# Performance work log

Measured on AMD Instinct MI355X. Metric: run time of the kernel, lower is better.

Reference implementation:

```python
import jax, jax.numpy as jnp
import numpy as np

B, T = 64, 512
E, F, NUM = 8, 64, 16          # num embedding features, per-feature emb dim, numeric feats
D = E * F + NUM                 # 528, input_dim
HE = 512                        # encoder_hidden
HD = 512                        # decoder_gru_hidden
V = 500                         # vocab per categorical feature


def setup_inputs() -> dict:
    key = jax.random.key(0)
    ks = jax.random.split(key, 32)
    se = 1.0 / np.sqrt(HE)
    sd = 1.0 / np.sqrt(HD)
    u = lambda k, shape, s: jax.random.uniform(k, shape, jnp.float32, -s, s)
    return dict(
        x=jax.random.normal(ks[0], (B, T, D), jnp.float32),
        # encoder nn.GRU params (gate order r,z,n)
        Wih=u(ks[1], (3 * HE, D), se), Whh=u(ks[2], (3 * HE, HE), se),
        bih=u(ks[3], (3 * HE,), se), bhh=u(ks[4], (3 * HE,), se),
        # decoder layer 0 (input_size=D)
        W0x=u(ks[5], (3 * HD, D), sd), b0x=u(ks[6], (3 * HD,), sd),
        W0h=u(ks[7], (3 * HD, HD), sd), b0h=u(ks[8], (3 * HD,), sd),
        W0m=u(ks[9], (HD, HE + HD), sd), b0m=u(ks[10], (HD,), sd),
        # decoder layer 1 (input_size=HD)
        W1x=u(ks[11], (3 * HD, HD), sd), b1x=u(ks[12], (3 * HD,), sd),
        W1h=u(ks[13], (3 * HD, HD), sd), b1h=u(ks[14], (3 * HD,), sd),
        W1m=u(ks[15], (HD, HE + HD), sd), b1m=u(ks[16], (HD,), sd),
        # output heads
        Wout=u(ks[17], (D, HD), sd), bout=u(ks[18], (D,), sd),
        Wdel=u(ks[19], (1, HD), sd), bdel=u(ks[20], (1,), sd),
        # stacked per-feature vocab heads: Linear(F, V) for each of E features
        Wemb=u(ks[21], (E, V, F), 1.0 / np.sqrt(F)), bemb=u(ks[22], (E, V), 1.0 / np.sqrt(F)),
        seq_lens=jax.random.randint(ks[23], (B,), 1, T + 1),
    )


def _gru_cell(xg, hg, hx):
    # xg, hg: [B, 3H] precomputed input/hidden projections; hx: mixed hidden
    xr, xz, xn = jnp.split(xg, 3, axis=-1)
    hr, hz, hn = jnp.split(hg, 3, axis=-1)
    r = jax.nn.sigmoid(xr + hr)
    z = jax.nn.sigmoid(xz + hz)
    n = jnp.tanh(xn + r * hn)
    return z * hx + (1.0 - z) * n  # custom GRUCell convention: hy = z*hx + (1-z)*n


def reference(x, Wih, Whh, bih, bhh, W0x, b0x, W0h, b0h, W0m, b0m,
              W1x, b1x, W1h, b1h, W1m, b1m, Wout, bout, Wdel, bdel,
              Wemb, bemb, seq_lens):
    Bc, Tc, Dc = x.shape
    # ---------------- encoder: standard nn.GRU ----------------
    xg_enc = jnp.einsum('btd,gd->tbg', x, Wih) + bih  # [T,B,3HE]

    def enc_step(h, xt):
        hg = h @ Whh.T + bhh
        xr, xz, xn = jnp.split(xt, 3, axis=-1)
        hr, hz, hn = jnp.split(hg, 3, axis=-1)
        r = jax.nn.sigmoid(xr + hr)
        z = jax.nn.sigmoid(xz + hz)
        n = jnp.tanh(xn + r * hn)
        h = (1.0 - z) * n + z * h  # torch nn.GRU convention
        return h, h

    _, hs = jax.lax.scan(enc_step, jnp.zeros((Bc, HE), x.dtype), xg_enc)  # hs: [T,B,HE]
    lens = jnp.clip(seq_lens - 1, 0, Tc - 1)
    last_hidden = hs[lens, jnp.arange(Bc)]  # == all_hid[:, lens].diagonal().T -> [B,HE]

    # ---------------- DecoderGRU with per-step global mixing ----------------
    x2h0 = jnp.einsum('btd,gd->tbg', x, W0x) + b0x  # [T,B,3HD]
    # mix_global(cat([global_hidden, hx])) : global part is constant over time
    ghm0 = last_hidden @ W0m[:, :HE].T + b0m  # [B,HD]
    ghm1 = last_hidden @ W1m[:, :HE].T + b1m
    W0mh = W0m[:, HE:]
    W1mh = W1m[:, HE:]

    def dec_step(carry, xg_t):
        h0, h1 = carry
        hx0 = ghm0 + h0 @ W0mh.T
        h0 = _gru_cell(xg_t, hx0 @ W0h.T + b0h, hx0)
        xg1 = h0 @ W1x.T + b1x
        hx1 = ghm1 + h1 @ W1mh.T
        h1 = _gru_cell(xg1, hx1 @ W1h.T + b1h, hx1)
        return (h0, h1), h1

    z0 = jnp.zeros((Bc, HD), x.dtype)
    _, dec = jax.lax.scan(dec_step, (z0, z0), x2h0)  # [T,B,HD]
    dec = dec.transpose(1, 0, 2)  # [B,T,HD]

    out = (dec @ Wout.T + bout)[:, :-1, :]              # [B,T-1,D]
    pred_delta = (dec @ Wdel.T + bdel)[:, :-1, 0]       # [B,T-1]
    resized = out[:, :, :E * F].reshape(Bc, Tc - 1, E, F)
    emb_logits = jnp.einsum('btef,evf->ebtv', resized, Wemb) + bemb[:, None, None, :]
    return out, pred_delta, emb_logits, last_hidden
```

## Files before the change

### kernel.cpp

```cpp
#include <hip/hip_runtime.h>
#include <stdint.h>

typedef unsigned short u16;
typedef __attribute__((ext_vector_type(8))) short short8;
typedef __attribute__((ext_vector_type(4))) float f32x4;

#define MFMA16(a,b,c) __builtin_amdgcn_mfma_f32_16x16x32_bf16((a),(b),(c),0,0,0)
#define AT_LD(p)    __hip_atomic_load((p), __ATOMIC_RELAXED, __HIP_MEMORY_SCOPE_AGENT)
#define AT_ST(p,v)  __hip_atomic_store((p), (v), __ATOMIC_RELAXED, __HIP_MEMORY_SCOPE_AGENT)

__device__ __forceinline__ float b2f(u16 u){
  union { uint32_t i; float f; } v; v.i = ((uint32_t)u) << 16; return v.f;
}
__device__ __forceinline__ u16 f2bf(float f){
  union { float f; uint32_t i; } v; v.f = f;
  uint32_t x = v.i;
  return (u16)((x + 0x7fffu + ((x >> 16) & 1u)) >> 16);
}
__device__ __forceinline__ float sigm(float x){ return 1.f/(1.f + __expf(-x)); }
__device__ __forceinline__ float tanh_f(float x){ float e = __expf(-2.f*x); return 2.f/(1.f+e) - 1.f; }

__device__ __forceinline__ void gbar_arrive(unsigned* flags, int my, unsigned target){
  __syncthreads();
  if (threadIdx.x == 0) AT_ST(&flags[my*32], target);
}
__device__ __forceinline__ void gbar_wait32(unsigned* flags, unsigned target){
  if (threadIdx.x < 32){
    while (AT_LD(&flags[threadIdx.x*32]) < target) {}
  }
  __syncthreads();
}
__device__ __forceinline__ void gbar_wait64(unsigned* flags, unsigned target){
  if (threadIdx.x < 64){
    while (AT_LD(&flags[threadIdx.x*32]) < target) {}
  }
  __syncthreads();
}

__device__ __forceinline__ f32x4 xpose4(f32x4 a, int m){
  int b0 = m & 1, b1 = (m >> 1) & 1;
  float s01 = b0 ? a[0] : a[1];
  float s23 = b0 ? a[2] : a[3];
  float r01 = __shfl_xor(s01, 1);
  float r23 = __shfl_xor(s23, 1);
  float w0 = b0 ? r01 : a[0];
  float w1 = b0 ? a[1] : r01;
  float w2 = b0 ? r23 : a[2];
  float w3 = b0 ? a[3] : r23;
  float u02 = b1 ? w0 : w2;
  float u13 = b1 ? w1 : w3;
  float p02 = __shfl_xor(u02, 2);
  float p13 = __shfl_xor(u13, 2);
  f32x4 x;
  x[0] = b1 ? p02 : w0;
  x[1] = b1 ? p13 : w1;
  x[2] = b1 ? w2 : p02;
  x[3] = b1 ? w3 : p13;
  return x;
}

__global__ void cvt_pad(const float* __restrict__ src, u16* __restrict__ dst,
                        int R, int sStride, int sOff, int Cd, int Ccopy){
  int i = blockIdx.x*256 + threadIdx.x;
  if (i >= R*Cd) return;
  int r = i / Cd, c = i % Cd;
  dst[i] = (c < Ccopy) ? f2bf(src[(size_t)r*sStride + sOff + c]) : (u16)0;
}

__global__ void padf(const float* __restrict__ src, float* __restrict__ dst, int R, int Cs, int Cd){
  int i = blockIdx.x*256 + threadIdx.x;
  if (i >= R*Cd) return;
  int r = i/Cd, c = i%Cd;
  dst[i] = (c < Cs) ? src[r*Cs + c] : 0.f;
}

__global__ void wmT_kernel(const float* __restrict__ Wm, u16* __restrict__ dst){
  int idx = blockIdx.x*256 + threadIdx.x;
  if (idx >= 512*512) return;
  int j = idx >> 9, k = idx & 511;
  dst[idx] = f2bf(Wm[(size_t)k*1024 + 512 + j]);
}

__global__ __launch_bounds__(256) void gemm_bt(
    const u16* __restrict__ A, int lda,
    const u16* __restrict__ Bw, int ldb,
    const float* __restrict__ bias,
    int M, int N, int K, int mode,
    void* __restrict__ o0, void* __restrict__ o1, void* __restrict__ o2, int ldo)
{
  if (mode == 3){
    int e = blockIdx.z;
    A    += (size_t)e * 64;
    Bw   += (size_t)e * 512 * 64;
    bias += (size_t)e * 512;
  }
  __shared__ u16 As[128*64];
  __shared__ u16 Bs[128*64];
  const int row0 = blockIdx.x * 128, col0 = blockIdx.y * 128;
  const int tid = threadIdx.x;
  const int l = tid & 63, w = tid >> 6;
  const int lr = l & 15, lk = l >> 4;
  const int wr = w >> 1, wc = w & 1;
  f32x4 acc[4][4];
  #pragma unroll
  for (int a=0;a<4;++a)
    #pragma unroll
    for (int b=0;b<4;++b) acc[a][b] = (f32x4){0.f,0.f,0.f,0.f};

  for (int k0 = 0; k0 < K; k0 += 64){
    #pragma unroll
    for (int s = 0; s < 4; ++s){
      int cid = s*256 + tid;
      int r = cid >> 3, ck = cid & 7;
      *(short8*)&As[r*64 + ck*8] = *(const short8*)&A[(size_t)(row0 + r)*lda + k0 + ck*8];
      *(short8*)&Bs[r*64 + ck*8] = *(const short8*)&Bw[(size_t)(col0 + r)*ldb + k0 + ck*8];
    }
    __syncthreads();
    #pragma unroll
    for (int kt = 0; kt < 2; ++kt){
      short8 af[4], bf[4];
      #pragma unroll
      for (int mt=0;mt<4;++mt) af[mt] = *(const short8*)&As[(wr*64 + mt*16 + lr)*64 + kt*32 + lk*8];
      #pragma unroll
      for (int nt=0;nt<4;++nt) bf[nt] = *(const short8*)&Bs[(wc*64 + nt*16 + lr)*64 + kt*32 + lk*8];
      #pragma unroll
      for (int mt=0;mt<4;++mt)
        #pragma unroll
        for (int nt=0;nt<4;++nt) acc[mt][nt] = MFMA16(af[mt], bf[nt], acc[mt][nt]);
    }
    __syncthreads();
  }

  #pragma unroll
  for (int mt=0;mt<4;++mt){
    #pragma unroll
    for (int nt=0;nt<4;++nt){
      int col = col0 + wc*64 + nt*16 + lr;
      float bv = bias[col];
      #pragma unroll
      for (int i=0;i<4;++i){
        int r = row0 + wr*64 + mt*16 + lk*4 + i;
        float v = acc[mt][nt][i] + bv;
        if (mode == 0){
          int bb = r >> 9, t = r & 511;
          size_t ro = ((size_t)t*64 + bb)*1536;
          if (col < 1536) ((u16*)o0)[ro + col] = f2bf(v);
          else            ((u16*)o1)[ro + col - 1536] = f2bf(v);
        } else if (mode == 1){
          ((u16*)o0)[(size_t)r*ldo + col] = f2bf(v);
        } else if (mode == 2){
          int t = r >> 6, bb = r & 63;
          if (t < 511){
            size_t orow = (size_t)bb*511 + t;
            if (col < 512){
              ((float*)o0)[orow*528 + col] = v;
              ((u16*)o2)[orow*512 + col] = f2bf(v);
            } else if (col < 528){
              ((float*)o0)[orow*528 + col] = v;
            } else if (col == 528){
              ((float*)o1)[orow] = v;
            }
          }
        } else if (mode == 3){
          if (r < M && col < 500) ((float*)o0)[(size_t)(blockIdx.z)*16352000ull + (size_t)r*500 + col] = v;
        } else {
          if (r < M) ((float*)o0)[(size_t)r*ldo + col] = v;
        }
      }
    }
  }
}

__global__ __launch_bounds__(256,1) void enc_kernel(
    const u16* __restrict__ Whh, const float* __restrict__ bhh,
    const u16* __restrict__ XGE, const int* __restrict__ seqs,
    u16* __restrict__ hd, float* __restrict__ lasth,
    unsigned* __restrict__ flags)
{
  __shared__ u16 hs[64*512];
  const int tid = threadIdx.x;
  const int l = tid & 63, w = tid >> 6;
  const int lr = l & 15, lk = l >> 4;
  const int m = l & 3;
  const int gw = blockIdx.x*4 + w;
  const int hcol = gw*4 + (lr >> 2);

  const int msel = (m == 3) ? 0 : m;
  const u16* wbase = Whh + ((size_t)(msel*512) + hcol)*512;
  short8 bw[16];
  #pragma unroll
  for (int kt=0;kt<16;++kt) bw[kt] = *(const short8*)&wbase[kt*32 + lk*8];

  const float bhr = bhh[hcol], bhz = bhh[512+hcol], bhn = bhh[1024+hcol];
  int rowc[4]; int len[4]; float hreg[4];
  float xr[4], xz[4], xn[4];
  #pragma unroll
  for (int c=0;c<4;++c){
    rowc[c] = c*16 + lk*4 + m;
    len[c] = seqs[rowc[c]];
    hreg[c] = 0.f;
    const u16* p = XGE + (size_t)rowc[c]*1536;
    xr[c]=b2f(p[hcol]); xz[c]=b2f(p[512+hcol]); xn[c]=b2f(p[1024+hcol]);
  }

  for (int t=0; t<512; ++t){
    const u16* hrd = hd + (t & 1)*32768;
    u16*       hwr = hd + ((t & 1)^1)*32768;
    const unsigned* h32 = (const unsigned*)hrd;
    #pragma unroll
    for (int cc=0; cc<16; ++cc){
      int S = cc*256 + tid;
      int row = S >> 6, s = S & 63;
      union { unsigned u[4]; short8 v; } pk;
      #pragma unroll
      for (int j=0;j<4;++j) pk.u[j] = AT_LD(h32 + S*4 + j);
      *(short8*)&hs[row*512 + ((s ^ (row&7))<<3)] = pk.v;
    }
    __syncthreads();
    #pragma unroll
    for (int c=0;c<4;++c){
      short8 af[16];
      #pragma unroll
      for (int kt=0;kt<16;++kt)
        af[kt] = *(const short8*)&hs[(c*16+lr)*512 + (((kt*4+lk) ^ (lr&7))<<3)];
      f32x4 acc = (f32x4){0.f,0.f,0.f,0.f};
      #pragma unroll
      for (int kt=0;kt<16;++kt) acc = MFMA16(af[kt], bw[kt], acc);
      f32x4 x = xpose4(acc, m);
      float rg = sigm(xr[c] + x[0] + bhr);
      float zg = sigm(xz[c] + x[1] + bhz);
      float ng = tanh_f(xn[c] + rg*(x[2] + bhn));
      float hv = (1.f - zg)*ng + zg*hreg[c];
      hreg[c] = hv;
      AT_ST(&hwr[rowc[c]*512 + hcol], f2bf(hv));
      if (t == len[c]-1) lasth[rowc[c]*512 + hcol] = hv;
    }
    if (t < 511){
      gbar_arrive(flags, blockIdx.x, (unsigned)(t+1));
      const u16* xgn = XGE + (size_t)(t+1)*98304;
      #pragma unroll
      for (int c=0;c<4;++c){
        const u16* p = xgn + (size_t)rowc[c]*1536;
        xr[c]=b2f(p[hcol]); xz[c]=b2f(p[512+hcol]); xn[c]=b2f(p[1024+hcol]);
      }
      gbar_wait32(flags, (unsigned)(t+1));
    }
  }
}

__global__ __launch_bounds__(256,1) void decf_kernel(
    const u16* __restrict__ Wm0, const u16* __restrict__ Wcp0,
    const float* __restrict__ ghm0v, const float* __restrict__ ghW0v,
    const u16* __restrict__ W1xc, const float* __restrict__ b1xv,
    const u16* __restrict__ Wm1, const u16* __restrict__ Wcp1,
    const float* __restrict__ ghm1v, const float* __restrict__ ghW1v,
    const u16* __restrict__ XG0,
    u16* __restrict__ h0d, u16* __restrict__ h1d,
    u16* __restrict__ xgb,
    u16* __restrict__ Hall,
    unsigned* __restrict__ flags)
{
  __shared__ u16 hs[64*512];
  const int tid = threadIdx.x;
  const int l = tid & 63, w = tid >> 6;
  const int lr = l & 15, lk = l >> 4;
  const int m = l & 3;
  const int role1 = (blockIdx.x >= 32) ? 1 : 0;
  const int b = blockIdx.x & 31;
  const int gw = b*4 + w;
  const int hcol = gw*4 + (lr >> 2);

  const u16* Wm  = role1 ? Wm1  : Wm0;
  const u16* Wcp = role1 ? Wcp1 : Wcp0;
  const float* ghm = role1 ? ghm1v : ghm0v;
  const float* ghW = role1 ? ghW1v : ghW0v;
  u16* hd = role1 ? h1d : h0d;

  const u16* wb = (m == 0) ? (Wm + (size_t)hcol*512)
                           : (Wcp + ((size_t)((m-1)*512) + hcol)*512);
  short8 bw[16];
  #pragma unroll
  for (int kt=0;kt<16;++kt) bw[kt] = *(const short8*)&wb[kt*32 + lk*8];

  const bool xact = (!role1) && (gw < 96);
  const int xcol0 = gw*16;
  const int cbase = xcol0 + (lr & ~3);
  short8 bwx[16];
  float bx0=0.f, bx1=0.f, bx2=0.f, bx3=0.f;
  if (xact){
    #pragma unroll
    for (int kt=0;kt<16;++kt) bwx[kt] = *(const short8*)&W1xc[(size_t)(xcol0+lr)*512 + kt*32 + lk*8];
    bx0 = b1xv[cbase]; bx1 = b1xv[cbase+1]; bx2 = b1xv[cbase+2]; bx3 = b1xv[cbase+3];
  }

  int rowc[4]; float ghmr[4], g0[4], g1[4], g2[4];
  #pragma unroll
  for (int c=0;c<4;++c){
    int row = c*16 + lk*4 + m; rowc[c] = row;
    ghmr[c] = ghm[row*512 + hcol];
    g0[c] = ghW[row*1536 + hcol];
    g1[c] = ghW[row*1536 + 512 + hcol];
    g2[c] = ghW[row*1536 + 1024 + hcol];
  }
  float xr[4], xz[4], xn[4];
  if (!role1){
    #pragma unroll
    for (int c=0;c<4;++c){
      const u16* p = XG0 + (size_t)rowc[c]*1536;
      xr[c]=b2f(p[hcol]); xz[c]=b2f(p[512+hcol]); xn[c]=b2f(p[1024+hcol]);
    }
  } else {
    #pragma unroll
    for (int c=0;c<4;++c){ xr[c]=0.f; xz[c]=0.f; xn[c]=0.f; }
  }

  for (int p=0; p<=513; ++p){
    if (!role1){
      if (p <= 512){
        const int sp = p & 1;
        const u16* hrd = h0d + sp*32768;
        u16*       hwr = h0d + (sp^1)*32768;
        const unsigned* h32 = (const unsigned*)hrd;
        #pragma unroll
        for (int cc=0; cc<16; ++cc){
          int S = cc*256 + tid;
          int row = S >> 6, s = S & 63;
          union { unsigned u[4]; short8 v; } pk;
          #pragma unroll
          for (int j=0;j<4;++j) pk.u[j] = AT_LD(h32 + S*4 + j);
          *(short8*)&hs[row*512 + ((s ^ (row&7))<<3)] = pk.v;
        }
        __syncthreads();
        u16* xw = xgb + (size_t)((p-1)&1)*98304;
        #pragma unroll
        for (int c=0;c<4;++c){
          short8 af[16];
          #pragma unroll
          for (int kt=0;kt<16;++kt)
            af[kt] = *(const short8*)&hs[(c*16+lr)*512 + (((kt*4+lk) ^ (lr&7))<<3)];
          if (p <= 511){
            f32x4 ga = (f32x4){0.f,0.f,0.f,0.f};
            #pragma unroll
            for (int kt=0;kt<16;++kt) ga = MFMA16(af[kt], bw[kt], ga);
            f32x4 x = xpose4(ga, m);
            float hx = x[0] + ghmr[c];
            float rv = sigm(xr[c] + x[1] + g0[c]);
            float zv = sigm(xz[c] + x[2] + g1[c]);
            float nv = tanh_f(xn[c] + rv*(x[3] + g2[c]));
            float hv = zv*hx + (1.f - zv)*nv;
            AT_ST(&hwr[rowc[c]*512 + hcol], f2bf(hv));
          }
          if (p >= 1 && xact){
            f32x4 xa = (f32x4){0.f,0.f,0.f,0.f};
            #pragma unroll
            for (int kt=0;kt<16;++kt) xa = MFMA16(af[kt], bwx[kt], xa);
            f32x4 xv = xpose4(xa, m);
            unsigned lo = (unsigned)f2bf(xv[0]+bx0) | ((unsigned)f2bf(xv[1]+bx1) << 16);
            unsigned hi = (unsigned)f2bf(xv[2]+bx2) | ((unsigned)f2bf(xv[3]+bx3) << 16);
            unsigned long long v64 = (unsigned long long)lo | ((unsigned long long)hi << 32);
            __hip_atomic_store((unsigned long long*)&xw[(size_t)rowc[c]*1536 + cbase], v64,
                               __ATOMIC_RELAXED, __HIP_MEMORY_SCOPE_AGENT);
          }
        }
      }
    } else {
      if (p >= 2){
        const int t = p - 2;
        const u16* xb = xgb + (size_t)(t&1)*98304;
        #pragma unroll
        for (int c=0;c<4;++c){
          xr[c] = b2f(AT_LD(&xb[(size_t)rowc[c]*1536 + hcol]));
          xz[c] = b2f(AT_LD(&xb[(size_t)rowc[c]*1536 + 512 + hcol]));
          xn[c] = b2f(AT_LD(&xb[(size_t)rowc[c]*1536 + 1024 + hcol]));
        }
        const u16* hrd = h1d + (t&1)*32768;
        u16*       hwr = h1d + ((t&1)^1)*32768;
        const unsigned* h32 = (const unsigned*)hrd;
        #pragma unroll
        for (int cc=0; cc<16; ++cc){
          int S = cc*256 + tid;
          int row = S >> 6, s = S & 63;
          union { unsigned u[4]; short8 v; } pk;
          #pragma unroll
          for (int j=0;j<4;++j) pk.u[j] = AT_LD(h32 + S*4 + j);
          *(short8*)&hs[row*512 + ((s ^ (row&7))<<3)] = pk.v;
        }
        __syncthreads();
        #pragma unroll
        for (int c=0;c<4;++c){
          short8 af[16];
          #pragma unroll
          for (int kt=0;kt<16;++kt)
            af[kt] = *(const short8*)&hs[(c*16+lr)*512 + (((kt*4+lk) ^ (lr&7))<<3)];
          f32x4 ga = (f32x4){0.f,0.f,0.f,0.f};
          #pragma unroll
          for (int kt=0;kt<16;++kt) ga = MFMA16(af[kt], bw[kt], ga);
          f32x4 x = xpose4(ga, m);
          float hx = x[0] + ghmr[c];
          float rv = sigm(xr[c] + x[1] + g0[c]);
          float zv = sigm(xz[c] + x[2] + g1[c]);
          float nv = tanh_f(xn[c] + rv*(x[3] + g2[c]));
          float hv = zv*hx + (1.f - zv)*nv;
          u16 hb = f2bf(hv);
          AT_ST(&hwr[rowc[c]*512 + hcol], hb);
          Hall[(size_t)t*32768 + rowc[c]*512 + hcol] = hb;
        }
      }
    }
    if (p < 513){
      gbar_arrive(flags, blockIdx.x, (unsigned)(p+1));
      if (!role1 && p <= 510){
        const u16* xgn = XG0 + (size_t)(p+1)*98304;
        #pragma unroll
        for (int c=0;c<4;++c){
          const u16* q = xgn + (size_t)rowc[c]*1536;
          xr[c]=b2f(q[hcol]); xz[c]=b2f(q[512+hcol]); xn[c]=b2f(q[1024+hcol]);
        }
      }
      gbar_wait64(flags, (unsigned)(p+1));
    }
  }
}

__global__ void ghm_kernel(const float* __restrict__ lasth,
                           const float* __restrict__ W0m, const float* __restrict__ b0m,
                           const float* __restrict__ W1m, const float* __restrict__ b1m,
                           float* __restrict__ ghm0, float* __restrict__ ghm1,
                           u16* __restrict__ ghmP)
{
  int idx = blockIdx.x*256 + threadIdx.x;
  int chain = idx >> 15;
  int j = (idx >> 6) & 511;
  int b = idx & 63;
  const float* Wm = chain ? W1m : W0m;
  const float* bm = chain ? b1m : b0m;
  float s = 0.f;
  for (int k=0;k<512;++k) s += lasth[b*512 + k] * Wm[(size_t)j*1024 + k];
  float v = s + bm[j];
  (chain ? ghm1 : ghm0)[b*512 + j] = v;
  ghmP[(size_t)chain*65536 + b*512 + j] = f2bf(v);
}

extern "C" void kernel_launch(void* const* d_in, const int* in_sizes, int n_in,
                              void* d_out, int out_size, void* d_ws, size_t ws_size,
                              hipStream_t stream)
{
  const float* x    = (const float*)d_in[0];
  const float* Wih  = (const float*)d_in[1];
  const float* Whh  = (const float*)d_in[2];
  const float* bih  = (const float*)d_in[3];
  const float* bhh  = (const float*)d_in[4];
  const float* W0x  = (const float*)d_in[5];
  const float* b0x  = (const float*)d_in[6];
  const float* W0h  = (const float*)d_in[7];
  const float* b0h  = (const float*)d_in[8];
  const float* W0m  = (const float*)d_in[9];
  const float* b0m  = (const float*)d_in[10];
  const float* W1x  = (const float*)d_in[11];
  const float* b1x  = (const float*)d_in[12];
  const float* W1h  = (const float*)d_in[13];
  const float* b1h  = (const float*)d_in[14];
  const float* W1m  = (const float*)d_in[15];
  const float* b1m  = (const float*)d_in[16];
  const float* Wout = (const float*)d_in[17];
  const float* bout = (const float*)d_in[18];
  const float* Wdel = (const float*)d_in[19];
  const float* bdel = (const float*)d_in[20];
  const float* Wemb = (const float*)d_in[21];
  const float* bemb = (const float*)d_in[22];
  const int*   seqs = (const int*)d_in[23];
  float* out = (float*)d_out;

  const size_t OFF_DELTA = 17267712ull;
  const size_t OFF_EMB   = 17300416ull;
  const size_t OFF_LASTH = 148116416ull;

  uint8_t* ws = (uint8_t*)d_ws;
  size_t off = 0;
  auto alloc = [&](size_t bytes)->size_t{ size_t p = off; off += (bytes + 511) & ~(size_t)511; return p; };
  u16*   XGE  = (u16*)(ws + alloc(32768ull*1536*2));
  u16*   WmT0 = XGE;
  u16*   WmT1 = XGE + 262144;
  u16*   XG0  = (u16*)(ws + alloc(32768ull*1536*2));
  u16*   Ob   = XG0;
  uint8_t* reg3 = ws + alloc(2ull*33554432);
  u16*   Xp   = (u16*)reg3;
  u16*   H1   = (u16*)reg3;
  u16*   Wc   = (u16*)(ws + alloc(3072ull*576*2));
  u16*   Whc  = (u16*)(ws + alloc(1536ull*512*2));
  u16*   W0hc = (u16*)(ws + alloc(1536ull*512*2));
  u16*   W1hc = (u16*)(ws + alloc(1536ull*512*2));
  u16*   W1xc = (u16*)(ws + alloc(1536ull*512*2));
  u16*   Wm0c = (u16*)(ws + alloc(512ull*512*2));
  u16*   Wm1c = (u16*)(ws + alloc(512ull*512*2));
  u16*   Wcp0 = (u16*)(ws + alloc(1536ull*512*2));
  u16*   Wcp1 = (u16*)(ws + alloc(1536ull*512*2));
  u16*   Woc  = (u16*)(ws + alloc(640ull*512*2));
  u16*   Wep  = (u16*)(ws + alloc(8ull*512*64*2));
  u16*   ghmP = (u16*)(ws + alloc(2ull*128*512*2));
  u16*   xgb  = (u16*)(ws + alloc(2ull*64*1536*2));
  float* bc1  = (float*)(ws + alloc(3072*4));
  float* bc3  = (float*)(ws + alloc(640*4));
  float* bep  = (float*)(ws + alloc(8*512*4));
  float* bzero= (float*)(ws + alloc(512*4));
  float* ghm0 = (float*)(ws + alloc(64*512*4));
  float* ghm1 = (float*)(ws + alloc(64*512*4));
  float* ghW0 = (float*)(ws + alloc(64*1536*4));
  float* ghW1 = (float*)(ws + alloc(64*1536*4));
  size_t state_off = off;
  u16*   henc = (u16*)(ws + alloc(2*64*512*2));
  u16*   h0d  = (u16*)(ws + alloc(2*64*512*2));
  u16*   h1d  = (u16*)(ws + alloc(2*64*512*2));
  unsigned* bars = (unsigned*)(ws + alloc(16384));
  size_t state_bytes = off - state_off;
  if (ws_size < off) return;

  hipMemsetAsync(ws + state_off, 0, state_bytes, stream);
  hipMemsetAsync(Woc, 0, 640ull*512*2, stream);
  hipMemsetAsync(Wep, 0, 8ull*512*64*2, stream);
  hipMemsetAsync(ghmP, 0, 2ull*128*512*2, stream);
  hipMemsetAsync(bc3, 0, 640*4, stream);
  hipMemsetAsync(bzero, 0, 512*4, stream);

  hipMemcpyAsync(bc1,        bih,  1536*4, hipMemcpyDeviceToDevice, stream);
  hipMemcpyAsync(bc1 + 1536, b0x,  1536*4, hipMemcpyDeviceToDevice, stream);
  hipMemcpyAsync(bc3,        bout, 528*4,  hipMemcpyDeviceToDevice, stream);
  hipMemcpyAsync(bc3 + 528,  bdel, 4,      hipMemcpyDeviceToDevice, stream);

  auto CV = [&](const float* s, u16* d, int R, int sStride, int sOff, int Cd, int Ccopy){
    int total = R*Cd; int gb = (total + 255)/256;
    cvt_pad<<<dim3(gb), dim3(256), 0, stream>>>(s, d, R, sStride, sOff, Cd, Ccopy);
  };
  CV(x,    Xp, 32768, 528, 0, 576, 528);
  CV(Wih,  Wc,              1536, 528, 0, 576, 528);
  CV(W0x,  Wc + 1536ull*576,1536, 528, 0, 576, 528);
  CV(Whh,  Whc,  1536, 512, 0, 512, 512);
  CV(W0h,  W0hc, 1536, 512, 0, 512, 512);
  CV(W1h,  W1hc, 1536, 512, 0, 512, 512);
  CV(W1x,  W1xc, 1536, 512, 0, 512, 512);
  CV(W0m,  Wm0c, 512, 1024, 512, 512, 512);
  CV(W1m,  Wm1c, 512, 1024, 512, 512, 512);
  CV(Wout, Woc,              528, 512, 0, 512, 512);
  CV(Wdel, Woc + 528ull*512, 1,   512, 0, 512, 512);
  for (int e=0;e<8;++e) CV(Wemb + (size_t)e*32000, Wep + (size_t)e*32768, 500, 64, 0, 64, 64);
  {
    int gb = (8*512 + 255)/256;
    padf<<<dim3(gb), dim3(256), 0, stream>>>(bemb, bep, 8, 500, 512);
  }
  wmT_kernel<<<dim3(1024), dim3(256), 0, stream>>>(W0m, WmT0);
  wmT_kernel<<<dim3(1024), dim3(256), 0, stream>>>(W1m, WmT1);

  gemm_bt<<<dim3(12,4), dim3(256), 0, stream>>>(W0hc, 512, WmT0, 512, bzero,
      1536, 512, 512, 1, Wcp0, nullptr, nullptr, 512);
  gemm_bt<<<dim3(12,4), dim3(256), 0, stream>>>(W1hc, 512, WmT1, 512, bzero,
      1536, 512, 512, 1, Wcp1, nullptr, nullptr, 512);

  gemm_bt<<<dim3(256,24), dim3(256), 0, stream>>>(Xp, 576, Wc, 576, bc1,
      32768, 3072, 576, 0, XGE, XG0, nullptr, 0);
  enc_kernel<<<dim3(32), dim3(256), 0, stream>>>(Whc, bhh, XGE, seqs,
      henc, out + OFF_LASTH, bars + 0);
  ghm_kernel<<<dim3(256), dim3(256), 0, stream>>>(out + OFF_LASTH, W0m, b0m, W1m, b1m,
      ghm0, ghm1, ghmP);
  gemm_bt<<<dim3(1,12), dim3(256), 0, stream>>>(ghmP, 512, W0hc, 512, b0h,
      64, 1536, 512, 5, ghW0, nullptr, nullptr, 1536);
  gemm_bt<<<dim3(1,12), dim3(256), 0, stream>>>(ghmP + 65536, 512, W1hc, 512, b1h,
      64, 1536, 512, 5, ghW1, nullptr, nullptr, 1536);
  decf_kernel<<<dim3(64), dim3(256), 0, stream>>>(
      Wm0c, Wcp0, ghm0, ghW0, W1xc, b1x,
      Wm1c, Wcp1, ghm1, ghW1,
      XG0, h0d, h1d, xgb, H1, bars + 1024);
  gemm_bt<<<dim3(256,5), dim3(256), 0, stream>>>(H1, 512, Woc, 512, bc3,
      32768, 640, 512, 2, out, out + OFF_DELTA, Ob, 0);
  gemm_bt<<<dim3(256,4,8), dim3(256), 0, stream>>>(Ob, 512, Wep, 64, bep,
      32704, 512, 64, 3, out + OFF_EMB, nullptr, nullptr, 0);
}
```

Baseline: 9.492 ms.

## Halve persistent recurrent blocks with 512 threads to cut grid-barrier participants

The encoder and decoder recurrent kernels now run 16/32 blocks of 512 threads (8 waves each) instead of 32/64 blocks of 256, so each global barrier polls half as many flags. Hidden-state staging into LDS uses 64-bit atomic loads through a shared helper, halving the load count. Each block stages the full hidden state once for twice as many columns, which reduces redundant L2 traffic. In exchange, per-block register pressure rises, and the fixed cost of the step loop is spread over fewer CUs.

```diff
diff --git a/kernel.cpp b/kernel.cpp
--- a/kernel.cpp
+++ b/kernel.cpp
@@ -7,6 +7,7 @@
 
 #define MFMA16(a,b,c) __builtin_amdgcn_mfma_f32_16x16x32_bf16((a),(b),(c),0,0,0)
 #define AT_LD(p)    __hip_atomic_load((p), __ATOMIC_RELAXED, __HIP_MEMORY_SCOPE_AGENT)
+#define AT_LD64(p)  __hip_atomic_load((p), __ATOMIC_RELAXED, __HIP_MEMORY_SCOPE_AGENT)
 #define AT_ST(p,v)  __hip_atomic_store((p), (v), __ATOMIC_RELAXED, __HIP_MEMORY_SCOPE_AGENT)
 
 __device__ __forceinline__ float b2f(u16 u){
@@ -24,14 +25,14 @@
   __syncthreads();
   if (threadIdx.x == 0) AT_ST(&flags[my*32], target);
 }
+__device__ __forceinline__ void gbar_wait16(unsigned* flags, unsigned target){
+  if (threadIdx.x < 16){
+    while (AT_LD(&flags[threadIdx.x*32]) < target) {}
+  }
+  __syncthreads();
+}
 __device__ __forceinline__ void gbar_wait32(unsigned* flags, unsigned target){
   if (threadIdx.x < 32){
-    while (AT_LD(&flags[threadIdx.x*32]) < target) {}
-  }
-  __syncthreads();
-}
-__device__ __forceinline__ void gbar_wait64(unsigned* flags, unsigned target){
-  if (threadIdx.x < 64){
     while (AT_LD(&flags[threadIdx.x*32]) < target) {}
   }
   __syncthreads();
@@ -57,6 +58,19 @@
   x[2] = b1 ? w2 : p02;
   x[3] = b1 ? w3 : p13;
   return x;
+}
+
+__device__ __forceinline__ void stage_h(const u16* hrd, u16* hs, int tid){
+  const unsigned long long* h64 = (const unsigned long long*)hrd;
+  #pragma unroll
+  for (int cc=0; cc<8; ++cc){
+    int S = cc*512 + tid;
+    int row = S >> 6, s = S & 63;
+    union { unsigned long long q[2]; short8 v; } pk;
+    pk.q[0] = AT_LD64(h64 + (size_t)S*2);
+    pk.q[1] = AT_LD64(h64 + (size_t)S*2 + 1);
+    *(short8*)&hs[row*512 + ((s ^ (row&7))<<3)] = pk.v;
+  }
 }
 
 __global__ void cvt_pad(const float* __restrict__ src, u16* __restrict__ dst,
@@ -171,7 +185,7 @@
   }
 }
 
-__global__ __launch_bounds__(256,1) void enc_kernel(
+__global__ __launch_bounds__(512,2) void enc_kernel(
     const u16* __restrict__ Whh, const float* __restrict__ bhh,
     const u16* __restrict__ XGE, const int* __restrict__ seqs,
     u16* __restrict__ hd, float* __restrict__ lasth,
@@ -182,7 +196,7 @@
   const int l = tid & 63, w = tid >> 6;
   const int lr = l & 15, lk = l >> 4;
   const int m = l & 3;
-  const int gw = blockIdx.x*4 + w;
+  const int gw = blockIdx.x*8 + w;
   const int hcol = gw*4 + (lr >> 2);
 
   const int msel = (m == 3) ? 0 : m;
@@ -206,16 +220,7 @@
   for (int t=0; t<512; ++t){
     const u16* hrd = hd + (t & 1)*32768;
     u16*       hwr = hd + ((t & 1)^1)*32768;
-    const unsigned* h32 = (const unsigned*)hrd;
-    #pragma unroll
-    for (int cc=0; cc<16; ++cc){
-      int S = cc*256 + tid;
-      int row = S >> 6, s = S & 63;
-      union { unsigned u[4]; short8 v; } pk;
-      #pragma unroll
-      for (int j=0;j<4;++j) pk.u[j] = AT_LD(h32 + S*4 + j);
-      *(short8*)&hs[row*512 + ((s ^ (row&7))<<3)] = pk.v;
-    }
+    stage_h(hrd, hs, tid);
     __syncthreads();
     #pragma unroll
     for (int c=0;c<4;++c){
@@ -243,12 +248,12 @@
         const u16* p = xgn + (size_t)rowc[c]*1536;
         xr[c]=b2f(p[hcol]); xz[c]=b2f(p[512+hcol]); xn[c]=b2f(p[1024+hcol]);
       }
-      gbar_wait32(flags, (unsigned)(t+1));
-    }
-  }
-}
-
-__global__ __launch_bounds__(256,1) void decf_kernel(
+      gbar_wait16(flags, (unsigned)(t+1));
+    }
+  }
+}
+
+__global__ __launch_bounds__(512,2) void decf_kernel(
     const u16* __restrict__ Wm0, const u16* __restrict__ Wcp0,
     const float* __restrict__ ghm0v, const float* __restrict__ ghW0v,
     const u16* __restrict__ W1xc, const float* __restrict__ b1xv,
@@ -265,16 +270,15 @@
   const int l = tid & 63, w = tid >> 6;
   const int lr = l & 15, lk = l >> 4;
   const int m = l & 3;
-  const int role1 = (blockIdx.x >= 32) ? 1 : 0;
-  const int b = blockIdx.x & 31;
-  const int gw = b*4 + w;
+  const int role1 = (blockIdx.x >= 16) ? 1 : 0;
+  const int b = blockIdx.x & 15;
+  const int gw = b*8 + w;
   const int hcol = gw*4 + (lr >> 2);
 
   const u16* Wm  = role1 ? Wm1  : Wm0;
   const u16* Wcp = role1 ? Wcp1 : Wcp0;
   const float* ghm = role1 ? ghm1v : ghm0v;
   const float* ghW = role1 ? ghW1v : ghW0v;
-  u16* hd = role1 ? h1d : h0d;
 
   const u16* wb = (m == 0) ? (Wm + (size_t)hcol*512)
                            : (Wcp + ((size_t)((m-1)*512) + hcol)*512);
@@ -320,16 +324,7 @@
         const int sp = p & 1;
         const u16* hrd = h0d + sp*32768;
         u16*       hwr = h0d + (sp^1)*32768;
-        const unsigned* h32 = (const unsigned*)hrd;
-        #pragma unroll
-        for (int cc=0; cc<16; ++cc){
-          int S = cc*256 + tid;
-          int row = S >> 6, s = S & 63;
-          union { unsigned u[4]; short8 v; } pk;
-          #pragma unroll
-          for (int j=0;j<4;++j) pk.u[j] = AT_LD(h32 + S*4 + j);
-          *(short8*)&hs[row*512 + ((s ^ (row&7))<<3)] = pk.v;
-        }
+        stage_h(hrd, hs, tid);
         __syncthreads();
         u16* xw = xgb + (size_t)((p-1)&1)*98304;
         #pragma unroll
@@ -375,16 +370,7 @@
         }
         const u16* hrd = h1d + (t&1)*32768;
         u16*       hwr = h1d + ((t&1)^1)*32768;
-        const unsigned* h32 = (const unsigned*)hrd;
-        #pragma unroll
-        for (int cc=0; cc<16; ++cc){
-          int S = cc*256 + tid;
-          int row = S >> 6, s = S & 63;
-          union { unsigned u[4]; short8 v; } pk;
-          #pragma unroll
-          for (int j=0;j<4;++j) pk.u[j] = AT_LD(h32 + S*4 + j);
-          *(short8*)&hs[row*512 + ((s ^ (row&7))<<3)] = pk.v;
-        }
+        stage_h(hrd, hs, tid);
         __syncthreads();
         #pragma unroll
         for (int c=0;c<4;++c){
@@ -417,7 +403,7 @@
           xr[c]=b2f(q[hcol]); xz[c]=b2f(q[512+hcol]); xn[c]=b2f(q[1024+hcol]);
         }
       }
-      gbar_wait64(flags, (unsigned)(p+1));
+      gbar_wait32(flags, (unsigned)(p+1));
     }
   }
 }
@@ -557,7 +543,7 @@
 
   gemm_bt<<<dim3(256,24), dim3(256), 0, stream>>>(Xp, 576, Wc, 576, bc1,
       32768, 3072, 576, 0, XGE, XG0, nullptr, 0);
-  enc_kernel<<<dim3(32), dim3(256), 0, stream>>>(Whc, bhh, XGE, seqs,
+  enc_kernel<<<dim3(16), dim3(512), 0, stream>>>(Whc, bhh, XGE, seqs,
       henc, out + OFF_LASTH, bars + 0);
   ghm_kernel<<<dim3(256), dim3(256), 0, stream>>>(out + OFF_LASTH, W0m, b0m, W1m, b1m,
       ghm0, ghm1, ghmP);
@@ -565,7 +551,7 @@
       64, 1536, 512, 5, ghW0, nullptr, nullptr, 1536);
   gemm_bt<<<dim3(1,12), dim3(256), 0, stream>>>(ghmP + 65536, 512, W1hc, 512, b1h,
       64, 1536, 512, 5, ghW1, nullptr, nullptr, 1536);
-  decf_kernel<<<dim3(64), dim3(256), 0, stream>>>(
+  decf_kernel<<<dim3(32), dim3(512), 0, stream>>>(
       Wm0c, Wcp0, ghm0, ghW0, W1xc, b1x,
       Wm1c, Wcp1, ghm1, ghW1,
       XG0, h0d, h1d, xgb, H1, bars + 1024);
```

Result: slower. 13.16 ms (+38.6%).
